# Performance work log

Measured on AMD Instinct MI355X. Metric: run time of the kernel, lower is better.

## Reference

```python
import jax, jax.numpy as jnp
import numpy as np

NEG_SLOPE = 0.1

def lrelu(x):
    return jnp.where(x >= 0, x, NEG_SLOPE * x)

def conv2d(x, w, b, padding=0, dilation=1):
    y = jax.lax.conv_general_dilated(
        x, w, window_strides=(1, 1),
        padding=[(padding, padding), (padding, padding)],
        rhs_dilation=(dilation, dilation),
        dimension_numbers=('NCHW', 'OIHW', 'NCHW'))
    return y + b[None, :, None, None]

def res_aspp(x, p):
    r1 = lrelu(conv2d(x, p['a1_w'], p['a1_b'], padding=1, dilation=1))
    r2 = lrelu(conv2d(x, p['a2_w'], p['a2_b'], padding=2, dilation=2))
    r3 = lrelu(conv2d(x, p['a3_w'], p['a3_b'], padding=4, dilation=4))
    r = conv2d(jnp.concatenate((r1, r2, r3), axis=1), p['ar_w'], p['ar_b'])
    return x + r

def deform_conv2d(x, offset, w, b):
    # x: [B,C,H,W], offset: [B,2*K,H,W] torchvision layout (y,x) per 3x3 tap
    B, C, H, W = x.shape
    KH = KW = 3
    K = KH * KW
    pad = 1
    off = offset.reshape(B, K, 2, H, W)
    ky, kx = jnp.meshgrid(jnp.arange(KH), jnp.arange(KW), indexing='ij')
    ky = ky.reshape(K).astype(x.dtype)
    kx = kx.reshape(K).astype(x.dtype)
    hh = jnp.arange(H, dtype=x.dtype)
    ww = jnp.arange(W, dtype=x.dtype)
    # sampling positions [B,K,H,W]
    py = off[:, :, 0] + (hh[None, None, :, None] - pad + ky[None, :, None, None])
    px = off[:, :, 1] + (ww[None, None, None, :] - pad + kx[None, :, None, None])
    y0 = jnp.floor(py)
    x0 = jnp.floor(px)
    wy = (py - y0)[:, None]  # [B,1,K,H,W]
    wx = (px - x0)[:, None]
    y0i = y0.astype(jnp.int32)
    x0i = x0.astype(jnp.int32)
    x_flat = x.reshape(B, C, H * W)

    def gather(iy, ix):
        valid = ((iy >= 0) & (iy < H) & (ix >= 0) & (ix < W)).astype(x.dtype)
        idx = jnp.clip(iy, 0, H - 1) * W + jnp.clip(ix, 0, W - 1)  # [B,K,H,W]
        v = jax.vmap(lambda xb, ib: xb[:, ib])(x_flat, idx.reshape(B, -1))
        return v.reshape(B, C, K, H, W) * valid[:, None]

    samp = (gather(y0i, x0i) * (1 - wy) * (1 - wx)
            + gather(y0i, x0i + 1) * (1 - wy) * wx
            + gather(y0i + 1, x0i) * wy * (1 - wx)
            + gather(y0i + 1, x0i + 1) * wy * wx)
    out = jnp.einsum('bckhw,ock->bohw', samp, w.reshape(w.shape[0], C, K))
    return out + b[None, :, None, None]

def setup_inputs() -> dict:
    key = jax.random.key(0)
    ks = jax.random.split(key, 16)
    B, C, H, W = 4, 64, 160, 160
    Cout = 64
    s = 0.05
    d = {
        'in_aux': jax.random.normal(ks[0], (B, C, H, W), jnp.float32),
        'in_ref': jax.random.normal(ks[1], (B, C, H, W), jnp.float32),
        'w01': jax.random.normal(ks[2], (Cout, 2 * C, 1, 1), jnp.float32) * s,
        'b01': jnp.zeros((Cout,), jnp.float32),
        'a1_w': jax.random.normal(ks[3], (Cout, Cout, 3, 3), jnp.float32) * s,
        'a1_b': jnp.zeros((Cout,), jnp.float32),
        'a2_w': jax.random.normal(ks[4], (Cout, Cout, 3, 3), jnp.float32) * s,
        'a2_b': jnp.zeros((Cout,), jnp.float32),
        'a3_w': jax.random.normal(ks[5], (Cout, Cout, 3, 3), jnp.float32) * s,
        'a3_b': jnp.zeros((Cout,), jnp.float32),
        'ar_w': jax.random.normal(ks[6], (Cout, 3 * Cout, 1, 1), jnp.float32) * s,
        'ar_b': jnp.zeros((Cout,), jnp.float32),
        'w02': jax.random.normal(ks[7], (18, Cout, 1, 1), jnp.float32) * s,
        'b02': jnp.zeros((18,), jnp.float32),
        'dw': jax.random.normal(ks[8], (Cout, C, 3, 3), jnp.float32) * s,
        'db': jnp.zeros((Cout,), jnp.float32),
    }
    return d

def reference(in_aux, in_ref, w01, b01, a1_w, a1_b, a2_w, a2_b, a3_w, a3_b,
              ar_w, ar_b, w02, b02, dw, db):
    cat_x = jnp.concatenate((in_aux, in_ref), axis=1)
    off_x = lrelu(conv2d(cat_x, w01, b01))
    p = {'a1_w': a1_w, 'a1_b': a1_b, 'a2_w': a2_w, 'a2_b': a2_b,
         'a3_w': a3_w, 'a3_b': a3_b, 'ar_w': ar_w, 'ar_b': ar_b}
    off_x = res_aspp(off_x, p)
    off_x = conv2d(off_x, w02, b02)
    return deform_conv2d(in_aux, off_x, dw, db)
```

## Files before the change

### kernel.cpp

```cpp
#include <hip/hip_runtime.h>
#include <math.h>

static constexpr int B = 4, H = 160, W = 160;
static constexpr int HW = H * W;
static constexpr int CHW = 64 * HW;
static constexpr int NELEM = B * CHW;

static constexpr int WP = 168;
static constexpr int HP = 168;
static constexpr int PHW = WP * HP;
static constexpr int PGUARD = 704;
static constexpr int PSTRIDE = 30720;
static constexpr int IMGOFS = PGUARD + 4 * WP + 4;

typedef short bf16x8 __attribute__((ext_vector_type(8)));
typedef float f32x4 __attribute__((ext_vector_type(4)));

__device__ __forceinline__ float lrelu(float v) { return v >= 0.f ? v : 0.1f * v; }

__device__ __forceinline__ unsigned short f2bf(float f) {
  unsigned u = __float_as_uint(f);
  return (unsigned short)((u + 0x7FFFu + ((u >> 16) & 1u)) >> 16);
}
__device__ __forceinline__ float bf2f(short u) {
  return __uint_as_float(((unsigned)(unsigned short)u) << 16);
}

__device__ __forceinline__ void glds16(const unsigned short* g, unsigned short* l) {
  __builtin_amdgcn_global_load_lds(
      (const __attribute__((address_space(1))) void*)g,
      (__attribute__((address_space(3))) void*)l, 16, 0, 0);
}

__global__ __launch_bounds__(256) void k_transform(
    const float* __restrict__ w01, const float* __restrict__ dw,
    const float* __restrict__ arw, const float* __restrict__ a1w,
    const float* __restrict__ a2w, const float* __restrict__ a3w,
    float* __restrict__ wt01, unsigned short* __restrict__ wb_bf,
    unsigned short* __restrict__ wd_bf, unsigned short* __restrict__ arw_bf,
    unsigned short* __restrict__ off0p) {
  int i = blockIdx.x * 256 + threadIdx.x;
  uint4* zp = (uint4*)off0p;
#pragma unroll
  for (int j = 0; j < 6; ++j) {
    unsigned u = (unsigned)i + (unsigned)j * 167936u;
    if (u < 983040u) zp[u] = make_uint4(0u, 0u, 0u, 0u);
  }
  if (i < 8192) {
    int ci = i >> 6, o = i & 63;
    wt01[i] = w01[o * 128 + ci];
  } else if (i < 118784) {
    int j = i - 8192;
    int ci = j & 63, co = (j >> 6) & 63;
    int kk = j >> 12;
    int dsel = kk / 9; kk -= dsel * 9;
    const float* src = dsel == 0 ? a1w : dsel == 1 ? a2w : a3w;
    wb_bf[j] = f2bf(src[(co * 64 + ci) * 9 + kk]);
  } else if (i < 155648) {
    int j = i - 118784;
    int ci = j & 63, co = (j >> 6) & 63, k = j >> 12;
    wd_bf[j] = f2bf(dw[(co * 64 + ci) * 9 + k]);
  } else if (i < 167936) {
    int j = i - 155648;
    arw_bf[j] = f2bf(arw[j]);
  }
}

__global__ __launch_bounds__(256) void k_conv1x1_in(
    const float* __restrict__ aux, const float* __restrict__ ref,
    const float* __restrict__ wt01, const float* __restrict__ b01,
    float* __restrict__ out, unsigned short* __restrict__ off0p,
    unsigned short* __restrict__ x_bf) {
  __shared__ float s[128 * 64];
  int pos0 = blockIdx.x * 64;
  int b = pos0 / HW;
  int hw0 = pos0 - b * HW;
  int tid = threadIdx.x;
  for (int i = tid; i < 8192; i += 256) {
    int ci = i >> 6, p = i & 63;
    const float* src = (ci < 64) ? (aux + b * CHW + ci * HW)
                                 : (ref + b * CHW + (ci - 64) * HW);
    s[i] = src[hw0 + p];
  }
  __syncthreads();
  int p = tid & 63;
  int g = __builtin_amdgcn_readfirstlane(tid >> 6);
  const float* wp = wt01 + g * 16;
  float acc[16];
#pragma unroll
  for (int j = 0; j < 16; ++j) acc[j] = 0.f;
#pragma unroll 4
  for (int ci = 0; ci < 128; ++ci) {
    float sv = s[ci * 64 + p];
    const float* wrow = wp + ci * 64;
#pragma unroll
    for (int j = 0; j < 16; ++j) acc[j] += sv * wrow[j];
  }
  const float* bb = b01 + g * 16;
  int obase = (b * 64 + g * 16) * HW + hw0 + p;
  unsigned short tb[16];
#pragma unroll
  for (int j = 0; j < 16; ++j) {
    float v = lrelu(acc[j] + bb[j]);
    out[obase + j * HW] = v;
    tb[j] = f2bf(v);
  }
  int hw = hw0 + p;
  int h = hw / W, w = hw - h * W;
  unsigned short* dst =
      off0p + ((size_t)b * PSTRIDE + IMGOFS + h * WP + w) * 64 + g * 16;
  *(uint4*)dst = *(const uint4*)&tb[0];
  *(uint4*)(dst + 8) = *(const uint4*)&tb[8];
  unsigned short xb[16];
#pragma unroll
  for (int j = 0; j < 16; ++j) xb[j] = f2bf(s[(g * 16 + j) * 64 + p]);
  unsigned short* xdst = x_bf + ((size_t)(b * HW + hw0 + p)) * 64 + g * 16;
  *(uint4*)xdst = *(const uint4*)&xb[0];
  *(uint4*)(xdst + 8) = *(const uint4*)&xb[8];
}

__global__ __launch_bounds__(256) void k_aspp3_mfma(
    const unsigned short* __restrict__ off0p,
    const unsigned short* __restrict__ wb_bf,
    const float* __restrict__ a1b, const float* __restrict__ a2b,
    const float* __restrict__ a3b, unsigned short* __restrict__ r_bf) {
  __shared__ unsigned short sa[256 * 72];
  int tid = threadIdx.x;
  int lane = tid & 63, wid = tid >> 6;
  int m = lane & 15, q = lane >> 4;

  int p0 = blockIdx.x;
  int xcd = p0 & 7, ii = p0 >> 3;
  int base = xcd < 4 ? xcd * 167 : 668 + (xcd - 4) * 166;
  int lid = base + ii;
  int dsel = lid % 3;
  int tj = lid / 3;
  int b = tj / 111;
  int tile = tj - b * 111;
  int pos0 = tile * 256;
  const int d = 1 << dsel;
  const unsigned short* pb = off0p + (size_t)b * PSTRIDE * 64;
  const float* bias = dsel == 0 ? a1b : dsel == 1 ? a2b : a3b;

  f32x4 acc[4][4] = {};
#pragma unroll
  for (int k9 = 0; k9 < 9; ++k9) {
    const int ky = k9 / 3, kx = k9 - ky * 3;
    const int ofs = ((ky - 1) * WP + (kx - 1)) * d;
    const unsigned short* src = pb + (size_t)(PGUARD + pos0 + ofs) * 64;
    __syncthreads();
#pragma unroll
    for (int r = 0; r < 8; ++r)
      glds16(src + r * 2048 + tid * 8, sa + r * 2048 + tid * 8);
    __syncthreads();
    const unsigned short* wk = wb_bf + (dsel * 9 + k9) * 4096;
#pragma unroll
    for (int kc = 0; kc < 2; ++kc) {
      bf16x8 bfrag[4];
#pragma unroll
      for (int t = 0; t < 4; ++t)
        bfrag[t] = *(const bf16x8*)(wk + (t * 16 + m) * 64 + kc * 32 + q * 8);
#pragma unroll
      for (int mt = 0; mt < 4; ++mt) {
        bf16x8 afrag =
            *(const bf16x8*)(sa + (wid * 64 + mt * 16 + m) * 64 + kc * 32 + q * 8);
#pragma unroll
        for (int t = 0; t < 4; ++t)
          acc[mt][t] = __builtin_amdgcn_mfma_f32_16x16x32_bf16(
              afrag, bfrag[t], acc[mt][t], 0, 0, 0);
      }
    }
  }

  __syncthreads();
#pragma unroll
  for (int t = 0; t < 4; ++t) {
    float bi = bias[t * 16 + m];
#pragma unroll
    for (int mt = 0; mt < 4; ++mt)
#pragma unroll
      for (int r = 0; r < 4; ++r)
        sa[(wid * 64 + mt * 16 + q * 4 + r) * 72 + t * 16 + m] =
            f2bf(lrelu(acc[mt][t][r] + bi));
  }
  __syncthreads();
  {
    int qa = pos0 + tid;
    int pr = qa / WP, pc = qa - pr * WP;
    if (pr >= 4 && pr < 164 && pc >= 4 && pc < 164) {
      int hw = (pr - 4) * W + (pc - 4);
      unsigned short* dst = r_bf + ((size_t)(b * HW + hw)) * 192 + dsel * 64;
      const unsigned short* s2 = sa + tid * 72;
#pragma unroll
      for (int c = 0; c < 8; ++c)
        *(uint4*)(dst + c * 8) = *(const uint4*)(s2 + c * 8);
    }
  }
}

__global__ __launch_bounds__(256) void k_merge_head_mfma(
    const unsigned short* __restrict__ r_bf, const float* __restrict__ off0,
    const unsigned short* __restrict__ arw_bf, const float* __restrict__ arb,
    const float* __restrict__ w02, const float* __restrict__ b02,
    float* __restrict__ offs) {
  __shared__ unsigned short sa[64 * 200];
  int pos0 = blockIdx.x * 64;
  int b = pos0 / HW;
  int hw0 = pos0 - b * HW;
  int tid = threadIdx.x;
  const unsigned short* gsrc = r_bf + (size_t)(b * HW + hw0) * 192;
  for (int i = tid; i < 1536; i += 256) {
    int pos = i / 24, c8 = i - pos * 24;
    *(uint4*)(sa + pos * 200 + c8 * 8) = *(const uint4*)(gsrc + i * 8);
  }
  __syncthreads();
  int lane = tid & 63, wid = tid >> 6;
  int m = lane & 15, q = lane >> 4;
  f32x4 acc[4] = {};
#pragma unroll
  for (int kc = 0; kc < 6; ++kc) {
    bf16x8 bfrag = *(const bf16x8*)(arw_bf + (wid * 16 + m) * 192 + kc * 32 + q * 8);
#pragma unroll
    for (int mt = 0; mt < 4; ++mt) {
      bf16x8 afrag = *(const bf16x8*)(sa + (mt * 16 + m) * 200 + kc * 32 + q * 8);
      acc[mt] = __builtin_amdgcn_mfma_f32_16x16x32_bf16(afrag, bfrag, acc[mt],
                                                        0, 0, 0);
    }
  }
  __syncthreads();
  float* ep = (float*)sa;
  int co = wid * 16 + m;
  float bi = arb[co];
  const float* resrow = off0 + (size_t)(b * 64 + co) * HW + hw0;
#pragma unroll
  for (int mt = 0; mt < 4; ++mt)
#pragma unroll
    for (int r = 0; r < 4; ++r) {
      int pos = mt * 16 + q * 4 + r;
      ep[pos * 65 + co] = acc[mt][r] + bi + resrow[pos];
    }
  __syncthreads();
  for (int i = tid; i < 1152; i += 256) {
    int t = i >> 6, p = i & 63;
    const float* w2 = w02 + t * 64;
    float o = b02[t];
#pragma unroll 8
    for (int c = 0; c < 64; ++c) o += ep[p * 65 + c] * w2[c];
    offs[(b * 18 + t) * HW + hw0 + p] = o;
  }
}

__global__ __launch_bounds__(256) void k_deform_mfma(
    const unsigned short* __restrict__ x_bf, const float* __restrict__ offs,
    const unsigned short* __restrict__ wd_bf, const float* __restrict__ db,
    float* __restrict__ out) {
  constexpr int SP = 72;
  __shared__ unsigned short sb[2][64 * SP];
  int blk = (blockIdx.x & 7) * 200 + (blockIdx.x >> 3);
  int pos0 = blk * 64;
  int b = pos0 / HW;
  int hw0 = pos0 - b * HW;
  int tid = threadIdx.x;
  int lane = tid & 63, wid = tid >> 6;
  int m = lane & 15, q = lane >> 4;
  int p = lane;
  int cg = wid;
  int hw = hw0 + p;
  int h = hw / W, wv = hw - h * W;
  const unsigned short* xb = x_bf + (size_t)b * HW * 64;
  const float* ob = offs + b * 18 * HW + hw;
  float offv[18];
#pragma unroll
  for (int j = 0; j < 18; ++j) offv[j] = ob[j * HW];
  f32x4 acc[4] = {};

#pragma unroll
  for (int k = 0; k < 9; ++k) {
    const int ky = k / 3, kx = k - ky * 3;
    float py = offv[2 * k] + (float)(h - 1 + ky);
    float px = offv[2 * k + 1] + (float)(wv - 1 + kx);
    float fy = floorf(py), fx = floorf(px);
    int iy0 = (int)fy, ix0 = (int)fx;
    float wy = py - fy, wx = px - fx;
    int iy1 = iy0 + 1, ix1 = ix0 + 1;
    float vy0 = (iy0 >= 0 && iy0 < H) ? 1.f : 0.f;
    float vy1 = (iy1 >= 0 && iy1 < H) ? 1.f : 0.f;
    float vx0 = (ix0 >= 0 && ix0 < W) ? 1.f : 0.f;
    float vx1 = (ix1 >= 0 && ix1 < W) ? 1.f : 0.f;
    int cy0 = min(max(iy0, 0), H - 1), cy1 = min(max(iy1, 0), H - 1);
    int cx0 = min(max(ix0, 0), W - 1), cx1 = min(max(ix1, 0), W - 1);
    float c00 = vy0 * vx0 * (1.f - wy) * (1.f - wx);
    float c01 = vy0 * vx1 * (1.f - wy) * wx;
    float c10 = vy1 * vx0 * wy * (1.f - wx);
    float c11 = vy1 * vx1 * wy * wx;
    const unsigned short* p00 = xb + (size_t)(cy0 * W + cx0) * 64 + cg * 16;
    const unsigned short* p01 = xb + (size_t)(cy0 * W + cx1) * 64 + cg * 16;
    const unsigned short* p10 = xb + (size_t)(cy1 * W + cx0) * 64 + cg * 16;
    const unsigned short* p11 = xb + (size_t)(cy1 * W + cx1) * 64 + cg * 16;
    unsigned short tb[16];
#pragma unroll
    for (int c2 = 0; c2 < 2; ++c2) {
      bf16x8 v00 = *(const bf16x8*)(p00 + c2 * 8);
      bf16x8 v01 = *(const bf16x8*)(p01 + c2 * 8);
      bf16x8 v10 = *(const bf16x8*)(p10 + c2 * 8);
      bf16x8 v11 = *(const bf16x8*)(p11 + c2 * 8);
#pragma unroll
      for (int j = 0; j < 8; ++j) {
        float sv = c00 * bf2f(v00[j]) + c01 * bf2f(v01[j]) +
                   c10 * bf2f(v10[j]) + c11 * bf2f(v11[j]);
        tb[c2 * 8 + j] = f2bf(sv);
      }
    }
    unsigned short* wr = &sb[k & 1][p * SP + cg * 16];
    *(uint4*)wr = *(const uint4*)&tb[0];
    *(uint4*)(wr + 8) = *(const uint4*)&tb[8];
    __syncthreads();
    const unsigned short* rb = &sb[k & 1][0];
#pragma unroll
    for (int kc = 0; kc < 2; ++kc) {
      bf16x8 bfrag =
          *(const bf16x8*)(wd_bf + (k * 64 + wid * 16 + m) * 64 + kc * 32 + q * 8);
#pragma unroll
      for (int mt = 0; mt < 4; ++mt) {
        bf16x8 afrag = *(const bf16x8*)(rb + (mt * 16 + m) * SP + kc * 32 + q * 8);
        acc[mt] = __builtin_amdgcn_mfma_f32_16x16x32_bf16(afrag, bfrag, acc[mt],
                                                          0, 0, 0);
      }
    }
  }
  int co = wid * 16 + m;
  float bias = db[co];
  size_t orow = (size_t)(b * 64 + co) * HW + hw0;
#pragma unroll
  for (int mt = 0; mt < 4; ++mt)
#pragma unroll
    for (int r = 0; r < 4; ++r)
      out[orow + mt * 16 + q * 4 + r] = acc[mt][r] + bias;
}

extern "C" void kernel_launch(void* const* d_in, const int* in_sizes, int n_in,
                              void* d_out, int out_size, void* d_ws, size_t ws_size,
                              hipStream_t stream) {
  const float* aux = (const float*)d_in[0];
  const float* ref = (const float*)d_in[1];
  const float* w01 = (const float*)d_in[2];
  const float* b01 = (const float*)d_in[3];
  const float* a1w = (const float*)d_in[4];
  const float* a1b = (const float*)d_in[5];
  const float* a2w = (const float*)d_in[6];
  const float* a2b = (const float*)d_in[7];
  const float* a3w = (const float*)d_in[8];
  const float* a3b = (const float*)d_in[9];
  const float* arw = (const float*)d_in[10];
  const float* arb = (const float*)d_in[11];
  const float* w02 = (const float*)d_in[12];
  const float* b02 = (const float*)d_in[13];
  const float* dw  = (const float*)d_in[14];
  const float* db  = (const float*)d_in[15];
  float* out = (float*)d_out;

  float* off0 = (float*)d_ws;
  float* offs = off0 + NELEM;
  float* wt01 = offs + B * 18 * HW;
  unsigned short* off0p = (unsigned short*)(wt01 + 8192);
  unsigned short* x_bf   = off0p + (size_t)B * PSTRIDE * 64;
  unsigned short* wb_bf  = x_bf + (size_t)NELEM;
  unsigned short* wd_bf  = wb_bf + 110592;
  unsigned short* arw_bf = wd_bf + 36864;
  unsigned short* r_bf   = arw_bf + 12288;

  k_transform<<<656, 256, 0, stream>>>(w01, dw, arw, a1w, a2w, a3w,
                                       wt01, wb_bf, wd_bf, arw_bf, off0p);
  k_conv1x1_in<<<B * HW / 64, 256, 0, stream>>>(aux, ref, wt01, b01, off0,
                                                off0p, x_bf);
  k_aspp3_mfma<<<1332, 256, 0, stream>>>(off0p, wb_bf, a1b, a2b, a3b, r_bf);
  k_merge_head_mfma<<<B * HW / 64, 256, 0, stream>>>(
      r_bf, off0, arw_bf, arb, w02, b02, offs);
  k_deform_mfma<<<B * HW / 64, 256, 0, stream>>>(x_bf, offs, wd_bf, db, out);
}
```

Baseline: 330.3 us.

## Stage one halo row per ky and double-buffer LDS in dilated ASPP conv

The dilated 3x3 ASPP kernel now loads one 288-pixel row span per kernel row (ky) into LDS and reuses it for all three kx taps by shifting the read offset. This cuts the nine separate tile loads to three. The loads are double-buffered so the next row's global-to-LDS copy overlaps the MFMA work on the current one. An XOR swizzle is applied to the LDS layout to avoid bank conflicts on fragment reads, and the epilogue row stride changes from 72 to 68. The cost is more LDS (two 288x64 buffers) and a fixed 16-pixel halo, which must cover the largest dilation of 4.

```diff
diff --git a/kernel.cpp b/kernel.cpp
--- a/kernel.cpp
+++ b/kernel.cpp
@@ -26,7 +26,7 @@
   return __uint_as_float(((unsigned)(unsigned short)u) << 16);
 }
 
-__device__ __forceinline__ void glds16(const unsigned short* g, unsigned short* l) {
+__device__ __forceinline__ void glds16(const void* g, void* l) {
   __builtin_amdgcn_global_load_lds(
       (const __attribute__((address_space(1))) void*)g,
       (__attribute__((address_space(3))) void*)l, 16, 0, 0);
@@ -124,7 +124,7 @@
     const unsigned short* __restrict__ wb_bf,
     const float* __restrict__ a1b, const float* __restrict__ a2b,
     const float* __restrict__ a3b, unsigned short* __restrict__ r_bf) {
-  __shared__ unsigned short sa[256 * 72];
+  __shared__ unsigned short sa[2][288 * 64];
   int tid = threadIdx.x;
   int lane = tid & 63, wid = tid >> 6;
   int m = lane & 15, q = lane >> 4;
@@ -143,36 +143,57 @@
   const float* bias = dsel == 0 ? a1b : dsel == 1 ? a2b : a3b;
 
   f32x4 acc[4][4] = {};
-#pragma unroll
-  for (int k9 = 0; k9 < 9; ++k9) {
-    const int ky = k9 / 3, kx = k9 - ky * 3;
-    const int ofs = ((ky - 1) * WP + (kx - 1)) * d;
-    const unsigned short* src = pb + (size_t)(PGUARD + pos0 + ofs) * 64;
-    __syncthreads();
-#pragma unroll
-    for (int r = 0; r < 8; ++r)
-      glds16(src + r * 2048 + tid * 8, sa + r * 2048 + tid * 8);
-    __syncthreads();
-    const unsigned short* wk = wb_bf + (dsel * 9 + k9) * 4096;
-#pragma unroll
-    for (int kc = 0; kc < 2; ++kc) {
-      bf16x8 bfrag[4];
-#pragma unroll
-      for (int t = 0; t < 4; ++t)
-        bfrag[t] = *(const bf16x8*)(wk + (t * 16 + m) * 64 + kc * 32 + q * 8);
-#pragma unroll
-      for (int mt = 0; mt < 4; ++mt) {
-        bf16x8 afrag =
-            *(const bf16x8*)(sa + (wid * 64 + mt * 16 + m) * 64 + kc * 32 + q * 8);
+
+  auto STAGE = [&](int buf, int ky) {
+    const char* src =
+        (const char*)(pb + (size_t)(PGUARD + pos0 + (ky - 1) * d * WP - 16) * 64);
+    char* dstb = (char*)&sa[buf][0];
+#pragma unroll
+    for (int r = 0; r < 9; ++r) {
+      int X = r * 4096 + tid * 16;
+      int row = X >> 7;
+      int Xs = X ^ ((row & 7) << 4);
+      glds16(src + Xs, dstb + X);
+    }
+  };
+  auto COMPUTE = [&](int buf, int ky) {
+    const char* sb = (const char*)&sa[buf][0];
+#pragma unroll
+    for (int kx = 0; kx < 3; ++kx) {
+      const unsigned short* wk = wb_bf + (dsel * 9 + ky * 3 + kx) * 4096;
+      int px0 = 16 + (kx - 1) * d + wid * 64;
+#pragma unroll
+      for (int kc = 0; kc < 2; ++kc) {
+        bf16x8 bfrag[4];
 #pragma unroll
         for (int t = 0; t < 4; ++t)
-          acc[mt][t] = __builtin_amdgcn_mfma_f32_16x16x32_bf16(
-              afrag, bfrag[t], acc[mt][t], 0, 0, 0);
+          bfrag[t] = *(const bf16x8*)(wk + (t * 16 + m) * 64 + kc * 32 + q * 8);
+#pragma unroll
+        for (int mt = 0; mt < 4; ++mt) {
+          int px = px0 + mt * 16 + m;
+          int byteoff = px * 128 + ((kc * 64 + q * 16) ^ ((px & 7) << 4));
+          bf16x8 afrag = *(const bf16x8*)(sb + byteoff);
+#pragma unroll
+          for (int t = 0; t < 4; ++t)
+            acc[mt][t] = __builtin_amdgcn_mfma_f32_16x16x32_bf16(
+                afrag, bfrag[t], acc[mt][t], 0, 0, 0);
+        }
       }
     }
-  }
-
-  __syncthreads();
+  };
+
+  STAGE(0, 0);
+  __syncthreads();
+  STAGE(1, 1);
+  COMPUTE(0, 0);
+  __syncthreads();
+  STAGE(0, 2);
+  COMPUTE(1, 1);
+  __syncthreads();
+  COMPUTE(0, 2);
+
+  __syncthreads();
+  unsigned short* epb = &sa[0][0];
 #pragma unroll
   for (int t = 0; t < 4; ++t) {
     float bi = bias[t * 16 + m];
@@ -180,7 +201,7 @@
     for (int mt = 0; mt < 4; ++mt)
 #pragma unroll
       for (int r = 0; r < 4; ++r)
-        sa[(wid * 64 + mt * 16 + q * 4 + r) * 72 + t * 16 + m] =
+        epb[(wid * 64 + mt * 16 + q * 4 + r) * 68 + t * 16 + m] =
             f2bf(lrelu(acc[mt][t][r] + bi));
   }
   __syncthreads();
@@ -190,7 +211,7 @@
     if (pr >= 4 && pr < 164 && pc >= 4 && pc < 164) {
       int hw = (pr - 4) * W + (pc - 4);
       unsigned short* dst = r_bf + ((size_t)(b * HW + hw)) * 192 + dsel * 64;
-      const unsigned short* s2 = sa + tid * 72;
+      const unsigned short* s2 = epb + tid * 68;
 #pragma unroll
       for (int c = 0; c < 8; ++c)
         *(uint4*)(dst + c * 8) = *(const uint4*)(s2 + c * 8);
```

Result: no change. 328.9 us (-0.4%).
